# Kernel optimization log

Measured on AMD Instinct MI355X. Metric: run time of the kernel, lower is better.

Reference implementation:

```python
import jax, jax.numpy as jnp
import numpy as np

B, N, D = 8, 2048, 192
G, S = 512, 32
OUT = 384
ALPHA, BETA = 1000.0, 100.0
EPS = 1e-05


def setup_inputs() -> dict:
    key = jax.random.key(0)
    ks = jax.random.split(key, 8)
    sc = 0.02
    return {
        "points": jax.random.normal(ks[0], (B, N, 3), jnp.float32),
        "feats": jax.random.normal(ks[1], (B, N, D), jnp.float32),
        # 1x1 conv weights (BN assumed folded, inference form)
        "W1": sc * jax.random.normal(ks[2], (OUT, 2 * D), jnp.float32),
        "b1": jnp.zeros((OUT,), jnp.float32),
        "Wa": sc * jax.random.normal(ks[3], (OUT // 2, OUT), jnp.float32),
        "ba": jnp.zeros((OUT // 2,), jnp.float32),
        "Wb": sc * jax.random.normal(ks[4], (OUT, OUT // 2), jnp.float32),
        "bb": jnp.zeros((OUT,), jnp.float32),
    }


def fps(pts, n_samples):
    """Farthest point sampling. pts: (B,N,3) -> idx (B,n_samples) int32."""
    def one(p):  # (N,3)
        def step(carry, _):
            dists, last = carry
            cur = p[last]                                 # (3,)
            d = jnp.sum((p - cur) ** 2, axis=-1)          # (N,)
            dists = jnp.minimum(dists, d)
            nxt = jnp.argmax(dists).astype(jnp.int32)
            return (dists, nxt), last
        init = (jnp.full((p.shape[0],), jnp.inf, p.dtype), jnp.int32(0))
        _, idxs = jax.lax.scan(step, init, None, length=n_samples)
        return idxs
    return jax.vmap(one)(pts)


def pairwise_sqdist(a, b):
    # a: (B,G,3), b: (B,N,3) -> (B,G,N)
    aa = jnp.sum(a * a, -1)[:, :, None]
    bb = jnp.sum(b * b, -1)[:, None, :]
    return aa + bb - 2.0 * jnp.einsum('bgd,bnd->bgn', a, b)


def group_points(x, idx):
    # x: (B,N,C), idx: (B,G,S) -> (B,G,S,C)
    return jax.vmap(lambda f, i: f[i])(x, idx)


def pos_embed(xyz):
    # xyz: (B,G,S,3) -> (B,G,S,OUT)  Fourier positional encoding
    in_dim = xyz.shape[-1]
    feat_dim = OUT // (2 * in_dim)
    freq = jnp.arange(feat_dim, dtype=xyz.dtype)
    denom = jnp.power(jnp.asarray(ALPHA, xyz.dtype), freq / feat_dim)
    z = BETA * xyz[..., None] / denom                      # (B,G,S,3,feat_dim)
    pos = jnp.concatenate([jnp.sin(z), jnp.cos(z)], axis=-1)
    return pos.reshape(*xyz.shape[:-1], OUT)


def _forward(points, feats, W1, b1, Wa, ba, Wb, bb):
    # FPS centers
    fps_idx = fps(points, G)                               # (B,G)
    centers = jax.vmap(lambda p, i: p[i])(points, fps_idx)  # (B,G,3)

    d2 = pairwise_sqdist(centers, points)                  # (B,G,N)
    _, knn_idx = jax.lax.top_k(-d2, S)                     # (B,G,S)

    neighbor_pts = group_points(points, knn_idx)           # (B,G,S,3)
    neighbor_feats = group_points(feats, knn_idx)          # (B,G,S,D)

    # 'sim' normalization: global (scalar, unbiased) std of centered neighbors
    diff = neighbor_pts - centers[:, :, None, :]
    m = jnp.mean(diff)
    std = jnp.sqrt(jnp.sum((diff - m) ** 2) / (diff.size - 1))
    neighbor_pts = diff / (std + EPS)

    # center feats via 1-NN of centers in points
    center_idx = jnp.argmin(d2, axis=-1)                   # (B,G)
    center_feats = jax.vmap(lambda f, i: f[i])(feats, center_idx)  # (B,G,D)

    # concat neighbor + broadcast center feats -> (B,G,S,2D)
    gf = jnp.concatenate(
        [neighbor_feats, jnp.broadcast_to(center_feats[:, :, None, :], (points.shape[0], G, S, D))],
        axis=-1)

    # shared MLP (1x1 conv) + ReLU
    gf = jax.nn.relu(jnp.einsum('bgsc,oc->bgso', gf, W1) + b1)  # (B,G,S,OUT)

    pos = pos_embed(neighbor_pts)                          # (B,G,S,OUT)
    gf = (gf + pos) * pos

    # residual block: conv(OUT->OUT/2)+ReLU, conv(OUT/2->OUT), +x, ReLU
    h = jax.nn.relu(jnp.einsum('bgso,ho->bgsh', gf, Wa) + ba)
    h = jnp.einsum('bgsh,oh->bgso', h, Wb) + bb
    gf = jax.nn.relu(h + gf)

    # fused max + mean pooling over neighbors (S)
    out = jnp.max(gf, axis=2) + jnp.mean(gf, axis=2)       # (B,G,OUT)
    return centers, out


def reference(points, feats, W1, b1, Wa, ba, Wb, bb):
    return _forward(points, feats, W1, b1, Wa, ba, Wb, bb)
```

## Files before the change

### kernel.cpp

```cpp
#include <hip/hip_runtime.h>
#include <math.h>

#define Bn   8
#define Nn   2048
#define Dn   192
#define Gn   512
#define Sn   32
#define OUTn 384
#define Mrows (Bn * Gn * Sn)

typedef __attribute__((ext_vector_type(8))) unsigned short ushortx8;
typedef __attribute__((ext_vector_type(8))) __bf16 bf16x8;
typedef __attribute__((ext_vector_type(4))) float floatx4;

static constexpr size_t OFF_KNN    = 0;
static constexpr size_t OFF_CIDX   = 524288;
static constexpr size_t OFF_DIFF   = 540672;
static constexpr size_t OFF_SUMS   = 2113536;
static constexpr size_t OFF_STD    = 2113552;
static constexpr size_t OFF_CNT    = 2113568;
static constexpr size_t OFF_DENOM  = 2113792;
static constexpr size_t OFF_W1B    = 2114048;
static constexpr size_t OFF_WAB    = 2408960;
static constexpr size_t OFF_WBB    = 2556416;
static constexpr size_t OFF_G1     = 2703872;
static constexpr size_t OFF_FEATB  = 103367168;
static constexpr size_t OFF_CSTAGE = 109658624;

__device__ __forceinline__ unsigned short f2bf(float f) {
  unsigned u = __float_as_uint(f);
  unsigned r = (u + 0x7FFFu + ((u >> 16) & 1u)) >> 16;
  return (unsigned short)r;
}
__device__ __forceinline__ float bf2f(unsigned short h) {
  return __uint_as_float(((unsigned)h) << 16);
}
__device__ __forceinline__ floatx4 mfma_bf16(ushortx8 a, ushortx8 b, floatx4 c) {
  return __builtin_amdgcn_mfma_f32_16x16x32_bf16(
      __builtin_bit_cast(bf16x8, a), __builtin_bit_cast(bf16x8, b), c, 0, 0, 0);
}

__device__ __forceinline__ void gld16(const void* g, void* l) {
  __builtin_amdgcn_global_load_lds(
      (const __attribute__((address_space(1))) unsigned int*)g,
      (__attribute__((address_space(3))) unsigned int*)l, 16, 0, 0);
}

template <int CTRL>
__device__ __forceinline__ float dpp_max(float v) {
  int o = __builtin_amdgcn_update_dpp(0, __float_as_int(v), CTRL, 0xf, 0xf, true);
  return fmaxf(v, __int_as_float(o));
}

__global__ __launch_bounds__(256) void fused_front_kernel(
    const float* __restrict__ points, float* __restrict__ centers,
    const float* __restrict__ W1, const float* __restrict__ Wa,
    const float* __restrict__ Wb, const float* __restrict__ feats,
    unsigned short* __restrict__ W1b, unsigned short* __restrict__ Wab,
    unsigned short* __restrict__ Wbb, unsigned short* __restrict__ featb,
    float* __restrict__ rdenomTab, float* __restrict__ cstage,
    int* __restrict__ knn, int* __restrict__ cidx, float* __restrict__ diffb,
    double* __restrict__ sums, int* __restrict__ cnt, float* __restrict__ stdp) {
  const int t = threadIdx.x;
  const int w = t >> 6, lane = t & 63;

  if (blockIdx.x >= 8 && blockIdx.x < 8 + 3360) {
    const int base = (blockIdx.x - 8) * 1024 + t;
#pragma unroll
    for (int j = 0; j < 4; ++j) {
      const int i = base + j * 256;
      if (i < 147456)        W1b[i] = f2bf(W1[i]);
      else if (i < 221184)   Wab[i - 147456] = f2bf(Wa[i - 147456]);
      else if (i < 294912)   Wbb[i - 221184] = f2bf(Wb[i - 221184]);
      else                   featb[i - 294912] = f2bf(feats[i - 294912]);
    }
    if (blockIdx.x == 8 && t < 64)
      rdenomTab[t] = (float)(1.0 / pow(1000.0, (double)t / 64.0));
    return;
  }

  if (blockIdx.x >= 8 + 3360) {
    const int bg = (blockIdx.x - 3368) * 4 + w;
    const int b = bg >> 9;
    const float* P = points + (size_t)b * Nn * 3;
    const unsigned* cs = (const unsigned*)(cstage + (size_t)bg * 3);

    unsigned ux, uy, uz;
    for (;;) {
      ux = __hip_atomic_load(cs + 0, __ATOMIC_RELAXED, __HIP_MEMORY_SCOPE_AGENT);
      uy = __hip_atomic_load(cs + 1, __ATOMIC_RELAXED, __HIP_MEMORY_SCOPE_AGENT);
      uz = __hip_atomic_load(cs + 2, __ATOMIC_RELAXED, __HIP_MEMORY_SCOPE_AGENT);
      if (ux != 0xFFFFFFFFu && uy != 0xFFFFFFFFu && uz != 0xFFFFFFFFu) break;
      __builtin_amdgcn_s_sleep(16);
    }
    const float cx = __uint_as_float(ux);
    const float cy = __uint_as_float(uy);
    const float cz = __uint_as_float(uz);
    const float aa = __fadd_rn(__fadd_rn(__fmul_rn(cx, cx), __fmul_rn(cy, cy)), __fmul_rn(cz, cz));

    unsigned key[32];
#pragma unroll 8
    for (int s = 0; s < 32; ++s) {
      const int n = s * 64 + lane;
      float X = P[n * 3], Y = P[n * 3 + 1], Z = P[n * 3 + 2];
      float bbv = __fadd_rn(__fadd_rn(__fmul_rn(X, X), __fmul_rn(Y, Y)), __fmul_rn(Z, Z));
      float dot = __fadd_rn(__fadd_rn(__fmul_rn(cx, X), __fmul_rn(cy, Y)), __fmul_rn(cz, Z));
      float d2 = __fsub_rn(__fadd_rn(aa, bbv), __fmul_rn(2.0f, dot));
      unsigned u = __float_as_uint(d2);
      key[s] = u ^ ((unsigned)((int)u >> 31) | 0x80000000u);
    }

    unsigned mk = key[0]; int ms = 0;
#pragma unroll
    for (int s = 1; s < 32; ++s)
      if (key[s] < mk) { mk = key[s]; ms = s; }

    int mysel = 0;
    for (int it = 0; it < Sn; ++it) {
      unsigned long long p = ((unsigned long long)mk << 32) | (unsigned)(ms * 64 + lane);
#pragma unroll
      for (int off = 1; off <= 32; off <<= 1) {
        unsigned long long o = __shfl_xor(p, off, 64);
        p = (o < p) ? o : p;
      }
      const int n_win = (int)(unsigned)p;
      if (lane == it) mysel = n_win;
      if (lane == (n_win & 63)) {
        const int sw = n_win >> 6;
#pragma unroll
        for (int s = 0; s < 32; ++s)
          if (s == sw) key[s] = 0xFFFFFFFFu;
        mk = key[0]; ms = 0;
#pragma unroll
        for (int s = 1; s < 32; ++s)
          if (key[s] < mk) { mk = key[s]; ms = s; }
      }
    }

    double s1 = 0.0, s2 = 0.0;
    if (lane < Sn) {
      knn[(size_t)bg * Sn + lane] = mysel;
      float X = P[mysel * 3], Y = P[mysel * 3 + 1], Z = P[mysel * 3 + 2];
      float dx = __fsub_rn(X, cx), dy = __fsub_rn(Y, cy), dz = __fsub_rn(Z, cz);
      float* db = diffb + (size_t)bg * 96 + lane * 3;
      db[0] = dx; db[1] = dy; db[2] = dz;
      s1 = (double)dx + (double)dy + (double)dz;
      s2 = (double)dx * (double)dx + (double)dy * (double)dy + (double)dz * (double)dz;
    }
#pragma unroll
    for (int off = 1; off <= 32; off <<= 1) {
      s1 += __shfl_xor(s1, off, 64);
      s2 += __shfl_xor(s2, off, 64);
    }
    if (lane == 0) {
      cidx[bg] = __shfl(mysel, 0, 64);
      atomicAdd(sums, s1);
      atomicAdd(sums + 1, s2);
    }
    __threadfence();
    __syncthreads();
    if (t == 0) {
      const int old = atomicAdd(cnt, 1);
      if (old == (Bn * Gn / 4) - 1) {
        __threadfence();
        const double S1 = atomicAdd(sums, 0.0);
        const double S2 = atomicAdd(sums + 1, 0.0);
        const double n = (double)(Bn * Gn * Sn * 3);
        const double mean = S1 / n;
        const double var = (S2 - S1 * mean) / (n - 1.0);
        const float stdf = (float)sqrt(var) + 1e-5f;
        *stdp = (float)(1.0 / (double)stdf);
      }
    }
    return;
  }

  const int b = blockIdx.x;
  __shared__ float4 p4[Nn];
  __shared__ unsigned long long wkey[2][4];

  const float* P = points + (size_t)b * Nn * 3;
  for (int n = t; n < Nn; n += 256) {
    float x = P[n * 3], y = P[n * 3 + 1], z = P[n * 3 + 2];
    p4[n] = make_float4(x, y, z, 0.f);
  }
  __syncthreads();

  float rx[8], ry[8], rz[8], dist[8];
#pragma unroll
  for (int k = 0; k < 8; ++k) {
    float4 p = p4[t * 8 + k];
    rx[k] = p.x; ry[k] = p.y; rz[k] = p.z;
    dist[k] = INFINITY;
  }

  int cur = 0;
  for (int it = 0; it < Gn; ++it) {
    const float4 c = p4[cur];
    if (t == 0) {
      float* cd = centers + ((size_t)b * Gn + it) * 3;
      cd[0] = c.x; cd[1] = c.y; cd[2] = c.z;
      unsigned* cs = (unsigned*)(cstage + ((size_t)b * Gn + it) * 3);
      __hip_atomic_store(cs + 0, __float_as_uint(c.x), __ATOMIC_RELAXED, __HIP_MEMORY_SCOPE_AGENT);
      __hip_atomic_store(cs + 1, __float_as_uint(c.y), __ATOMIC_RELAXED, __HIP_MEMORY_SCOPE_AGENT);
      __hip_atomic_store(cs + 2, __float_as_uint(c.z), __ATOMIC_RELAXED, __HIP_MEMORY_SCOPE_AGENT);
    }
    float bv = -1.0f;
#pragma unroll
    for (int k = 0; k < 8; ++k) {
      float dx = __fsub_rn(rx[k], c.x);
      float dy = __fsub_rn(ry[k], c.y);
      float dz = __fsub_rn(rz[k], c.z);
      float d = __fadd_rn(__fadd_rn(__fmul_rn(dx, dx), __fmul_rn(dy, dy)), __fmul_rn(dz, dz));
      dist[k] = fminf(dist[k], d);
      bv = fmaxf(bv, dist[k]);
    }
    int li = 7;
#pragma unroll
    for (int k = 6; k >= 0; --k) li = (dist[k] == bv) ? k : li;

    float red = bv;
    red = dpp_max<0x111>(red);
    red = dpp_max<0x112>(red);
    red = dpp_max<0x114>(red);
    red = dpp_max<0x118>(red);
    red = dpp_max<0x142>(red);
    red = dpp_max<0x143>(red);
    const float M = __int_as_float(__builtin_amdgcn_readlane(__float_as_int(red), 63));

    unsigned long long msk = __ballot(bv == M);
    const int L = __ffsll((long long)msk) - 1;
    const int liL = __builtin_amdgcn_readlane(li, L);
    const int idx = (w * 64 + L) * 8 + liL;

    unsigned long long key =
        ((unsigned long long)__float_as_uint(M) << 32) | (unsigned)(0x7FFFFFFF - idx);
    if (lane == 0) wkey[it & 1][w] = key;
    __syncthreads();
    unsigned long long k0 = wkey[it & 1][0];
    unsigned long long k1 = wkey[it & 1][1];
    unsigned long long k2 = wkey[it & 1][2];
    unsigned long long k3 = wkey[it & 1][3];
    unsigned long long m01 = (k1 > k0) ? k1 : k0;
    unsigned long long m23 = (k3 > k2) ? k3 : k2;
    unsigned long long mm = (m23 > m01) ? m23 : m01;
    cur = 0x7FFFFFFF - (int)(unsigned)mm;
  }
}

__global__ __launch_bounds__(256) void gemm1_kernel(
    const unsigned short* __restrict__ featb, const unsigned short* __restrict__ W1b,
    const float* __restrict__ b1, const int* __restrict__ knn,
    const int* __restrict__ cidx, const float* __restrict__ diffb,
    const float* __restrict__ rstd_p, const float* __restrict__ rdenomTab,
    unsigned short* __restrict__ G1) {
  __shared__ unsigned short As[128 * 64];
  __shared__ unsigned short Bs[128 * 64];
  const int t = threadIdx.x;
  const int bm = blockIdx.x, bn = blockIdx.y;
  const int wid = t >> 6, lane = t & 63, quad = lane >> 4, c16 = lane & 15;
  const int wr = wid >> 1, wc = wid & 1;

  int aOffN[4], aOffC[4], bOff[4];
#pragma unroll
  for (int i = 0; i < 4; ++i) {
    const int slot = i * 256 + t;
    const int row = slot >> 3, segV = slot & 7;
    const int seg = segV ^ (row & 7);
    const int grow = bm * 128 + row;
    const int bg = grow >> 5, s = grow & 31, bb_ = bg >> 9;
    const int nidx = knn[(size_t)bg * Sn + s];
    const int ci = cidx[bg];
    aOffN[i] = (bb_ * Nn + nidx) * Dn + seg * 8;
    aOffC[i] = (bb_ * Nn + ci) * Dn + seg * 8;
    bOff[i] = (bn * 128 + row) * 384 + seg * 8;
  }

  floatx4 acc[4][4];
#pragma unroll
  for (int i = 0; i < 4; ++i)
#pragma unroll
    for (int j = 0; j < 4; ++j) acc[i][j] = (floatx4){0.f, 0.f, 0.f, 0.f};

  for (int kt = 0; kt < 6; ++kt) {
    const int kb = kt * 64;
#pragma unroll
    for (int i = 0; i < 4; ++i) {
      const unsigned short* srcA =
          (kt < 3) ? (featb + aOffN[i] + kb) : (featb + aOffC[i] + (kb - 192));
      gld16(srcA, &As[(i * 256 + wid * 64) * 8]);
      gld16(W1b + bOff[i] + kb, &Bs[(i * 256 + wid * 64) * 8]);
    }
    __syncthreads();
#pragma unroll
    for (int ks = 0; ks < 2; ++ks) {
      ushortx8 af[4], bf[4];
#pragma unroll
      for (int mt = 0; mt < 4; ++mt) {
        const int row = wr * 64 + mt * 16 + c16;
        const int seg = (ks * 4 + quad) ^ (row & 7);
        af[mt] = *(const ushortx8*)&As[row * 64 + seg * 8];
      }
#pragma unroll
      for (int nt = 0; nt < 4; ++nt) {
        const int row = wc * 64 + nt * 16 + c16;
        const int seg = (ks * 4 + quad) ^ (row & 7);
        bf[nt] = *(const ushortx8*)&Bs[row * 64 + seg * 8];
      }
#pragma unroll
      for (int mt = 0; mt < 4; ++mt)
#pragma unroll
        for (int nt = 0; nt < 4; ++nt)
          acc[mt][nt] = mfma_bf16(af[mt], bf[nt], acc[mt][nt]);
    }
    __syncthreads();
  }

  const float rstd = *rstd_p;
  float bias[4], rdnm[4];
  bool usin[4];
#pragma unroll
  for (int nt = 0; nt < 4; ++nt) {
    const int col = bn * 128 + wc * 64 + nt * 16 + c16;
    bias[nt] = b1[col];
    const int j = col & 127;
    usin[nt] = (j < 64);
    rdnm[nt] = rdenomTab[j & 63];
  }
#pragma unroll
  for (int mt = 0; mt < 4; ++mt) {
#pragma unroll
    for (int r = 0; r < 4; ++r) {
      const int row = bm * 128 + wr * 64 + mt * 16 + quad * 4 + r;
      const float dv = diffb[(size_t)row * 3 + bn];
      const float x = __fmul_rn(dv, rstd);
      const float zb = __fmul_rn(100.0f, x);
#pragma unroll
      for (int nt = 0; nt < 4; ++nt) {
        const int col = bn * 128 + wc * 64 + nt * 16 + c16;
        float y = fmaxf(acc[mt][nt][r] + bias[nt], 0.f);
        float z = __fmul_rn(zb, rdnm[nt]);
        float p = usin[nt] ? __sinf(z) : __cosf(z);
        float g = (y + p) * p;
        G1[(size_t)row * 384 + col] = f2bf(g);
      }
    }
  }
}

__global__ __launch_bounds__(512) void gemm23_kernel(
    const unsigned short* __restrict__ G1, const unsigned short* __restrict__ Wab,
    const float* __restrict__ ba, const unsigned short* __restrict__ Wbb,
    const float* __restrict__ bb, float* __restrict__ outp) {
  __shared__ __align__(16) char smem[100352];
  unsigned short* Htile = (unsigned short*)smem;
  unsigned short* As    = (unsigned short*)(smem + 51200);
  unsigned short* BsA   = (unsigned short*)(smem + 51200 + 16384);
  unsigned short* BsB   = (unsigned short*)(smem + 51200);

  const int t = threadIdx.x;
  const int bm = blockIdx.x;
  const int lane = t & 63, quad = lane >> 4, c16 = lane & 15;
  const int wid = t >> 6;
  const int wr = wid >> 2, wc = wid & 3;

  int aOff[2], bOffA[3];
#pragma unroll
  for (int i = 0; i < 2; ++i) {
    const int slot = i * 512 + t;
    const int row = slot >> 3, segV = slot & 7;
    aOff[i] = (bm * 128 + row) * 384 + (segV ^ (row & 7)) * 8;
  }
#pragma unroll
  for (int i = 0; i < 3; ++i) {
    const int slot = i * 512 + t;
    const int row = slot >> 3, segV = slot & 7;
    bOffA[i] = row * 384 + (segV ^ (row & 7)) * 8;
  }

  floatx4 accA[4][3];
#pragma unroll
  for (int i = 0; i < 4; ++i)
#pragma unroll
    for (int j = 0; j < 3; ++j) accA[i][j] = (floatx4){0.f, 0.f, 0.f, 0.f};

  for (int kt = 0; kt < 6; ++kt) {
    const int kb = kt * 64;
#pragma unroll
    for (int i = 0; i < 2; ++i) gld16(G1 + aOff[i] + kb, As + ((size_t)(i * 512 + t)) * 8);
#pragma unroll
    for (int i = 0; i < 3; ++i) gld16(Wab + bOffA[i] + kb, BsA + ((size_t)(i * 512 + t)) * 8);
    __syncthreads();
#pragma unroll
    for (int ks = 0; ks < 2; ++ks) {
      ushortx8 af[4], bf[3];
#pragma unroll
      for (int mt = 0; mt < 4; ++mt) {
        const int row = wr * 64 + mt * 16 + c16;
        const int seg = (ks * 4 + quad) ^ (row & 7);
        af[mt] = *(const ushortx8*)&As[row * 64 + seg * 8];
      }
#pragma unroll
      for (int nt = 0; nt < 3; ++nt) {
        const int row = wc * 48 + nt * 16 + c16;
        const int seg = (ks * 4 + quad) ^ (row & 7);
        bf[nt] = *(const ushortx8*)&BsA[row * 64 + seg * 8];
      }
#pragma unroll
      for (int mt = 0; mt < 4; ++mt)
#pragma unroll
        for (int nt = 0; nt < 3; ++nt)
          accA[mt][nt] = mfma_bf16(af[mt], bf[nt], accA[mt][nt]);
    }
    __syncthreads();
  }

#pragma unroll
  for (int nt = 0; nt < 3; ++nt) {
    const int col = wc * 48 + nt * 16 + c16;
    const float bias = ba[col];
#pragma unroll
    for (int mt = 0; mt < 4; ++mt)
#pragma unroll
      for (int r = 0; r < 4; ++r) {
        const int row = wr * 64 + mt * 16 + quad * 4 + r;
        Htile[row * 200 + col] = f2bf(fmaxf(accA[mt][nt][r] + bias, 0.f));
      }
  }
  __syncthreads();

  int bOffB[6];
#pragma unroll
  for (int i = 0; i < 6; ++i) {
    const int slot = i * 512 + t;
    const int row = slot >> 3, segV = slot & 7;
    bOffB[i] = row * 192 + (segV ^ (row & 7)) * 8;
  }

  floatx4 acc[4][6];
#pragma unroll
  for (int i = 0; i < 4; ++i)
#pragma unroll
    for (int j = 0; j < 6; ++j) acc[i][j] = (floatx4){0.f, 0.f, 0.f, 0.f};

  for (int kt = 0; kt < 3; ++kt) {
    const int kb = kt * 64;
#pragma unroll
    for (int i = 0; i < 6; ++i) gld16(Wbb + bOffB[i] + kb, BsB + ((size_t)(i * 512 + t)) * 8);
    __syncthreads();
#pragma unroll
    for (int ks = 0; ks < 2; ++ks) {
      ushortx8 af[4], bf[6];
#pragma unroll
      for (int mt = 0; mt < 4; ++mt) {
        const int row = wr * 64 + mt * 16 + c16;
        af[mt] = *(const ushortx8*)&Htile[row * 200 + kb + ks * 32 + quad * 8];
      }
#pragma unroll
      for (int nt = 0; nt < 6; ++nt) {
        const int row = wc * 96 + nt * 16 + c16;
        const int seg = (ks * 4 + quad) ^ (row & 7);
        bf[nt] = *(const ushortx8*)&BsB[row * 64 + seg * 8];
      }
#pragma unroll
      for (int mt = 0; mt < 4; ++mt)
#pragma unroll
        for (int nt = 0; nt < 6; ++nt)
          acc[mt][nt] = mfma_bf16(af[mt], bf[nt], acc[mt][nt]);
    }
    __syncthreads();
  }

#pragma unroll
  for (int nt = 0; nt < 6; ++nt) {
    const int col = wc * 96 + nt * 16 + c16;
    const float bias = bb[col];
    float gmax[2] = {-INFINITY, -INFINITY};
    float gsum[2] = {0.f, 0.f};
#pragma unroll
    for (int mt = 0; mt < 4; ++mt) {
      const int grp = mt >> 1;
#pragma unroll
      for (int r = 0; r < 4; ++r) {
        const int row = bm * 128 + wr * 64 + mt * 16 + quad * 4 + r;
        float v = acc[mt][nt][r] + bias + bf2f(G1[(size_t)row * 384 + col]);
        v = fmaxf(v, 0.f);
        gmax[grp] = fmaxf(gmax[grp], v);
        gsum[grp] += v;
      }
    }
#pragma unroll
    for (int grp = 0; grp < 2; ++grp) {
      float m = gmax[grp], su = gsum[grp];
#pragma unroll
      for (int off = 16; off <= 32; off <<= 1) {
        m = fmaxf(m, __shfl_xor(m, off, 64));
        su += __shfl_xor(su, off, 64);
      }
      if (quad == 0) {
        const int bg = bm * 4 + wr * 2 + grp;
        outp[(size_t)bg * 384 + col] = m + su / 32.0f;
      }
    }
  }
}

extern "C" void kernel_launch(void* const* d_in, const int* in_sizes, int n_in,
                              void* d_out, int out_size, void* d_ws, size_t ws_size,
                              hipStream_t stream) {
  const float* points = (const float*)d_in[0];
  const float* feats  = (const float*)d_in[1];
  const float* W1 = (const float*)d_in[2];
  const float* b1 = (const float*)d_in[3];
  const float* Wa = (const float*)d_in[4];
  const float* ba = (const float*)d_in[5];
  const float* Wb = (const float*)d_in[6];
  const float* bb = (const float*)d_in[7];
  float* outF = (float*)d_out;

  char* ws = (char*)d_ws;
  int*            knn      = (int*)(ws + OFF_KNN);
  int*            cidx     = (int*)(ws + OFF_CIDX);
  float*          diffb    = (float*)(ws + OFF_DIFF);
  double*         sums     = (double*)(ws + OFF_SUMS);
  float*          stdp     = (float*)(ws + OFF_STD);
  int*            cnt      = (int*)(ws + OFF_CNT);
  float*          rdenomTab= (float*)(ws + OFF_DENOM);
  unsigned short* W1b      = (unsigned short*)(ws + OFF_W1B);
  unsigned short* Wab      = (unsigned short*)(ws + OFF_WAB);
  unsigned short* Wbb      = (unsigned short*)(ws + OFF_WBB);
  unsigned short* G1       = (unsigned short*)(ws + OFF_G1);
  unsigned short* featb    = (unsigned short*)(ws + OFF_FEATB);
  float*          cstage   = (float*)(ws + OFF_CSTAGE);

  hipMemsetAsync(ws + OFF_SUMS, 0, 40, stream);
  hipMemsetAsync(ws + OFF_CSTAGE, 0xFF, (size_t)Bn * Gn * 3 * 4, stream);
  fused_front_kernel<<<8 + 3360 + 1024, 256, 0, stream>>>(
      points, outF, W1, Wa, Wb, feats, W1b, Wab, Wbb, featb, rdenomTab,
      cstage, knn, cidx, diffb, sums, cnt, stdp);
  gemm1_kernel<<<dim3(Mrows / 128, 3), 256, 0, stream>>>(featb, W1b, b1, knn, cidx,
                                                         diffb, stdp, rdenomTab, G1);
  gemm23_kernel<<<Mrows / 128, 512, 0, stream>>>(G1, Wab, ba, Wbb, bb, outF + Bn * Gn * 3);
}
```

Baseline: 459.8 us.

## Fuse gemm1 into front mega-kernel with flag-based producer/consumer sync

The separate gemm1 kernel becomes a third role inside the front kernel. GEMM1 tiles spin on per-group completion flags from the kNN blocks and on a prep-done counter, so their matrix work can overlap the serial FPS and kNN phases. The normalization step still waits for a global std value, which is published with a release store. The bf16 conversion prep is also vectorized to pack two values per 32-bit store, halving its block count. The cost is spin-waiting blocks holding CU slots, and correctness now depends on blocks being dispatched in index order to avoid deadlock.

```diff
diff --git a/kernel.cpp b/kernel.cpp
--- a/kernel.cpp
+++ b/kernel.cpp
@@ -9,6 +9,14 @@
 #define OUTn 384
 #define Mrows (Bn * Gn * Sn)
 
+#define NB_FPS   8
+#define NB_PREP  1680
+#define NB_KNN   1024
+#define NB_G1    3072
+#define BLK_PREP (NB_FPS)
+#define BLK_KNN  (NB_FPS + NB_PREP)
+#define BLK_G1   (NB_FPS + NB_PREP + NB_KNN)
+
 typedef __attribute__((ext_vector_type(8))) unsigned short ushortx8;
 typedef __attribute__((ext_vector_type(8))) __bf16 bf16x8;
 typedef __attribute__((ext_vector_type(4))) float floatx4;
@@ -19,6 +27,7 @@
 static constexpr size_t OFF_SUMS   = 2113536;
 static constexpr size_t OFF_STD    = 2113552;
 static constexpr size_t OFF_CNT    = 2113568;
+static constexpr size_t OFF_PCNT   = 2113572;
 static constexpr size_t OFF_DENOM  = 2113792;
 static constexpr size_t OFF_W1B    = 2114048;
 static constexpr size_t OFF_WAB    = 2408960;
@@ -26,6 +35,7 @@
 static constexpr size_t OFF_G1     = 2703872;
 static constexpr size_t OFF_FEATB  = 103367168;
 static constexpr size_t OFF_CSTAGE = 109658624;
+static constexpr size_t OFF_GFLAG  = 109707776;
 
 __device__ __forceinline__ unsigned short f2bf(float f) {
   unsigned u = __float_as_uint(f);
@@ -39,57 +49,80 @@
   return __builtin_amdgcn_mfma_f32_16x16x32_bf16(
       __builtin_bit_cast(bf16x8, a), __builtin_bit_cast(bf16x8, b), c, 0, 0, 0);
 }
-
 __device__ __forceinline__ void gld16(const void* g, void* l) {
   __builtin_amdgcn_global_load_lds(
       (const __attribute__((address_space(1))) unsigned int*)g,
       (__attribute__((address_space(3))) unsigned int*)l, 16, 0, 0);
 }
-
 template <int CTRL>
 __device__ __forceinline__ float dpp_max(float v) {
   int o = __builtin_amdgcn_update_dpp(0, __float_as_int(v), CTRL, 0xf, 0xf, true);
   return fmaxf(v, __int_as_float(o));
 }
-
-__global__ __launch_bounds__(256) void fused_front_kernel(
+__device__ __forceinline__ void ast_u32(unsigned* p, unsigned v) {
+  __hip_atomic_store(p, v, __ATOMIC_RELAXED, __HIP_MEMORY_SCOPE_AGENT);
+}
+__device__ __forceinline__ void ast_f32(float* p, float v) {
+  __hip_atomic_store(p, v, __ATOMIC_RELAXED, __HIP_MEMORY_SCOPE_AGENT);
+}
+__device__ __forceinline__ unsigned ald_u32(const unsigned* p) {
+  return __hip_atomic_load(p, __ATOMIC_RELAXED, __HIP_MEMORY_SCOPE_AGENT);
+}
+
+__global__ __launch_bounds__(256) void mega_kernel(
     const float* __restrict__ points, float* __restrict__ centers,
     const float* __restrict__ W1, const float* __restrict__ Wa,
     const float* __restrict__ Wb, const float* __restrict__ feats,
+    const float* __restrict__ b1,
     unsigned short* __restrict__ W1b, unsigned short* __restrict__ Wab,
     unsigned short* __restrict__ Wbb, unsigned short* __restrict__ featb,
     float* __restrict__ rdenomTab, float* __restrict__ cstage,
     int* __restrict__ knn, int* __restrict__ cidx, float* __restrict__ diffb,
-    double* __restrict__ sums, int* __restrict__ cnt, float* __restrict__ stdp) {
+    double* __restrict__ sums, int* __restrict__ cnt, unsigned* __restrict__ stdbits,
+    unsigned* __restrict__ pcnt, unsigned* __restrict__ gflag,
+    unsigned short* __restrict__ G1) {
   const int t = threadIdx.x;
   const int w = t >> 6, lane = t & 63;
-
-  if (blockIdx.x >= 8 && blockIdx.x < 8 + 3360) {
-    const int base = (blockIdx.x - 8) * 1024 + t;
+  const int blk = blockIdx.x;
+  __shared__ __align__(16) char smem[32832];
+
+  if (blk >= BLK_PREP && blk < BLK_KNN) {
+    unsigned* W1b32 = (unsigned*)W1b;
+    unsigned* Wab32 = (unsigned*)Wab;
+    unsigned* Wbb32 = (unsigned*)Wbb;
+    unsigned* fb32  = (unsigned*)featb;
+    const int base = (blk - BLK_PREP) * 1024 + t;
 #pragma unroll
     for (int j = 0; j < 4; ++j) {
       const int i = base + j * 256;
-      if (i < 147456)        W1b[i] = f2bf(W1[i]);
-      else if (i < 221184)   Wab[i - 147456] = f2bf(Wa[i - 147456]);
-      else if (i < 294912)   Wbb[i - 221184] = f2bf(Wb[i - 221184]);
-      else                   featb[i - 294912] = f2bf(feats[i - 294912]);
-    }
-    if (blockIdx.x == 8 && t < 64)
-      rdenomTab[t] = (float)(1.0 / pow(1000.0, (double)t / 64.0));
+      const float* src; unsigned* dst; int k;
+      if (i < 73728)       { src = W1;    dst = W1b32; k = i; }
+      else if (i < 110592) { src = Wa;    dst = Wab32; k = i - 73728; }
+      else if (i < 147456) { src = Wb;    dst = Wbb32; k = i - 110592; }
+      else                 { src = feats; dst = fb32;  k = i - 147456; }
+      const unsigned lo = f2bf(src[2 * k]);
+      const unsigned hi = f2bf(src[2 * k + 1]);
+      ast_u32(dst + k, lo | (hi << 16));
+    }
+    if (blk == BLK_PREP && t < 64)
+      ast_f32(rdenomTab + t, (float)(1.0 / pow(1000.0, (double)t / 64.0)));
+    __syncthreads();
+    if (t == 0) {
+      __threadfence();
+      __hip_atomic_fetch_add(pcnt, 1u, __ATOMIC_RELEASE, __HIP_MEMORY_SCOPE_AGENT);
+    }
     return;
   }
 
-  if (blockIdx.x >= 8 + 3360) {
-    const int bg = (blockIdx.x - 3368) * 4 + w;
+  if (blk >= BLK_KNN && blk < BLK_G1) {
+    const int bg = (blk - BLK_KNN) * 4 + w;
     const int b = bg >> 9;
     const float* P = points + (size_t)b * Nn * 3;
     const unsigned* cs = (const unsigned*)(cstage + (size_t)bg * 3);
 
     unsigned ux, uy, uz;
     for (;;) {
-      ux = __hip_atomic_load(cs + 0, __ATOMIC_RELAXED, __HIP_MEMORY_SCOPE_AGENT);
-      uy = __hip_atomic_load(cs + 1, __ATOMIC_RELAXED, __HIP_MEMORY_SCOPE_AGENT);
-      uz = __hip_atomic_load(cs + 2, __ATOMIC_RELAXED, __HIP_MEMORY_SCOPE_AGENT);
+      ux = ald_u32(cs + 0); uy = ald_u32(cs + 1); uz = ald_u32(cs + 2);
       if (ux != 0xFFFFFFFFu && uy != 0xFFFFFFFFu && uz != 0xFFFFFFFFu) break;
       __builtin_amdgcn_s_sleep(16);
     }
@@ -109,7 +142,6 @@
       unsigned u = __float_as_uint(d2);
       key[s] = u ^ ((unsigned)((int)u >> 31) | 0x80000000u);
     }
-
     unsigned mk = key[0]; int ms = 0;
 #pragma unroll
     for (int s = 1; s < 32; ++s)
@@ -139,11 +171,11 @@
 
     double s1 = 0.0, s2 = 0.0;
     if (lane < Sn) {
-      knn[(size_t)bg * Sn + lane] = mysel;
+      ast_u32((unsigned*)&knn[(size_t)bg * Sn + lane], (unsigned)mysel);
       float X = P[mysel * 3], Y = P[mysel * 3 + 1], Z = P[mysel * 3 + 2];
       float dx = __fsub_rn(X, cx), dy = __fsub_rn(Y, cy), dz = __fsub_rn(Z, cz);
       float* db = diffb + (size_t)bg * 96 + lane * 3;
-      db[0] = dx; db[1] = dy; db[2] = dz;
+      ast_f32(db + 0, dx); ast_f32(db + 1, dy); ast_f32(db + 2, dz);
       s1 = (double)dx + (double)dy + (double)dz;
       s2 = (double)dx * (double)dx + (double)dy * (double)dy + (double)dz * (double)dz;
     }
@@ -153,15 +185,16 @@
       s2 += __shfl_xor(s2, off, 64);
     }
     if (lane == 0) {
-      cidx[bg] = __shfl(mysel, 0, 64);
+      ast_u32((unsigned*)&cidx[bg], (unsigned)__shfl(mysel, 0, 64));
       atomicAdd(sums, s1);
       atomicAdd(sums + 1, s2);
+      __hip_atomic_store(&gflag[bg], 1u, __ATOMIC_RELEASE, __HIP_MEMORY_SCOPE_AGENT);
     }
     __threadfence();
     __syncthreads();
     if (t == 0) {
       const int old = atomicAdd(cnt, 1);
-      if (old == (Bn * Gn / 4) - 1) {
+      if (old == NB_KNN - 1) {
         __threadfence();
         const double S1 = atomicAdd(sums, 0.0);
         const double S2 = atomicAdd(sums + 1, 0.0);
@@ -169,15 +202,129 @@
         const double mean = S1 / n;
         const double var = (S2 - S1 * mean) / (n - 1.0);
         const float stdf = (float)sqrt(var) + 1e-5f;
-        *stdp = (float)(1.0 / (double)stdf);
+        const float rstdv = (float)(1.0 / (double)stdf);
+        __hip_atomic_store(stdbits, __float_as_uint(rstdv), __ATOMIC_RELEASE,
+                           __HIP_MEMORY_SCOPE_AGENT);
       }
     }
     return;
   }
 
-  const int b = blockIdx.x;
-  __shared__ float4 p4[Nn];
-  __shared__ unsigned long long wkey[2][4];
+  if (blk >= BLK_G1) {
+    const int gb = blk - BLK_G1;
+    const int bm = gb & 1023, bn = gb >> 10;
+    unsigned short* As = (unsigned short*)smem;
+    unsigned short* Bs = (unsigned short*)(smem + 16384);
+    const int wid = w, quad = lane >> 4, c16 = lane & 15;
+    const int wr = wid >> 1, wc = wid & 1;
+
+    while (__hip_atomic_load(pcnt, __ATOMIC_ACQUIRE, __HIP_MEMORY_SCOPE_AGENT) <
+           (unsigned)NB_PREP)
+      __builtin_amdgcn_s_sleep(32);
+#pragma unroll
+    for (int g = 0; g < 4; ++g)
+      while (__hip_atomic_load(&gflag[bm * 4 + g], __ATOMIC_ACQUIRE,
+                               __HIP_MEMORY_SCOPE_AGENT) == 0u)
+        __builtin_amdgcn_s_sleep(16);
+
+    int aOffN[4], aOffC[4], bOff[4];
+#pragma unroll
+    for (int i = 0; i < 4; ++i) {
+      const int slot = i * 256 + t;
+      const int row = slot >> 3, segV = slot & 7;
+      const int seg = segV ^ (row & 7);
+      const int grow = bm * 128 + row;
+      const int bg = grow >> 5, s = grow & 31, bb_ = bg >> 9;
+      const int nidx = knn[(size_t)bg * Sn + s];
+      const int ci = (int)ald_u32((const unsigned*)&cidx[bg]);
+      aOffN[i] = (bb_ * Nn + nidx) * Dn + seg * 8;
+      aOffC[i] = (bb_ * Nn + ci) * Dn + seg * 8;
+      bOff[i] = (bn * 128 + row) * 384 + seg * 8;
+    }
+
+    floatx4 acc[4][4];
+#pragma unroll
+    for (int i = 0; i < 4; ++i)
+#pragma unroll
+      for (int j = 0; j < 4; ++j) acc[i][j] = (floatx4){0.f, 0.f, 0.f, 0.f};
+
+    for (int kt = 0; kt < 6; ++kt) {
+      const int kb = kt * 64;
+#pragma unroll
+      for (int i = 0; i < 4; ++i) {
+        const unsigned short* srcA =
+            (kt < 3) ? (featb + aOffN[i] + kb) : (featb + aOffC[i] + (kb - 192));
+        gld16(srcA, &As[(i * 256 + wid * 64) * 8]);
+        gld16(W1b + bOff[i] + kb, &Bs[(i * 256 + wid * 64) * 8]);
+      }
+      __syncthreads();
+#pragma unroll
+      for (int ks = 0; ks < 2; ++ks) {
+        ushortx8 af[4], bf[4];
+#pragma unroll
+        for (int mt = 0; mt < 4; ++mt) {
+          const int row = wr * 64 + mt * 16 + c16;
+          const int seg = (ks * 4 + quad) ^ (row & 7);
+          af[mt] = *(const ushortx8*)&As[row * 64 + seg * 8];
+        }
+#pragma unroll
+        for (int nt = 0; nt < 4; ++nt) {
+          const int row = wc * 64 + nt * 16 + c16;
+          const int seg = (ks * 4 + quad) ^ (row & 7);
+          bf[nt] = *(const ushortx8*)&Bs[row * 64 + seg * 8];
+        }
+#pragma unroll
+        for (int mt = 0; mt < 4; ++mt)
+#pragma unroll
+          for (int nt = 0; nt < 4; ++nt)
+            acc[mt][nt] = mfma_bf16(af[mt], bf[nt], acc[mt][nt]);
+      }
+      __syncthreads();
+    }
+
+    unsigned sb;
+    for (;;) {
+      sb = __hip_atomic_load(stdbits, __ATOMIC_ACQUIRE, __HIP_MEMORY_SCOPE_AGENT);
+      if (sb != 0xFFFFFFFFu) break;
+      __builtin_amdgcn_s_sleep(16);
+    }
+    const float rstd = __uint_as_float(sb);
+
+    float bias[4], rdnm[4];
+    bool usin[4];
+#pragma unroll
+    for (int nt = 0; nt < 4; ++nt) {
+      const int col = bn * 128 + wc * 64 + nt * 16 + c16;
+      bias[nt] = b1[col];
+      const int j = col & 127;
+      usin[nt] = (j < 64);
+      rdnm[nt] = rdenomTab[j & 63];
+    }
+#pragma unroll
+    for (int mt = 0; mt < 4; ++mt) {
+#pragma unroll
+      for (int r = 0; r < 4; ++r) {
+        const int row = bm * 128 + wr * 64 + mt * 16 + quad * 4 + r;
+        const float dv = diffb[(size_t)row * 3 + bn];
+        const float x = __fmul_rn(dv, rstd);
+        const float zb = __fmul_rn(100.0f, x);
+#pragma unroll
+        for (int nt = 0; nt < 4; ++nt) {
+          const int col = bn * 128 + wc * 64 + nt * 16 + c16;
+          float y = fmaxf(acc[mt][nt][r] + bias[nt], 0.f);
+          float z = __fmul_rn(zb, rdnm[nt]);
+          float p = usin[nt] ? __sinf(z) : __cosf(z);
+          float g = (y + p) * p;
+          G1[(size_t)row * 384 + col] = f2bf(g);
+        }
+      }
+    }
+    return;
+  }
+
+  const int b = blk;
+  float4* p4 = (float4*)smem;
+  unsigned long long* wkey = (unsigned long long*)(smem + 32768);
 
   const float* P = points + (size_t)b * Nn * 3;
   for (int n = t; n < Nn; n += 256) {
@@ -201,9 +348,9 @@
       float* cd = centers + ((size_t)b * Gn + it) * 3;
       cd[0] = c.x; cd[1] = c.y; cd[2] = c.z;
       unsigned* cs = (unsigned*)(cstage + ((size_t)b * Gn + it) * 3);
-      __hip_atomic_store(cs + 0, __float_as_uint(c.x), __ATOMIC_RELAXED, __HIP_MEMORY_SCOPE_AGENT);
-      __hip_atomic_store(cs + 1, __float_as_uint(c.y), __ATOMIC_RELAXED, __HIP_MEMORY_SCOPE_AGENT);
-      __hip_atomic_store(cs + 2, __float_as_uint(c.z), __ATOMIC_RELAXED, __HIP_MEMORY_SCOPE_AGENT);
+      ast_u32(cs + 0, __float_as_uint(c.x));
+      ast_u32(cs + 1, __float_as_uint(c.y));
+      ast_u32(cs + 2, __float_as_uint(c.z));
     }
     float bv = -1.0f;
 #pragma unroll
@@ -235,116 +382,16 @@
 
     unsigned long long key =
         ((unsigned long long)__float_as_uint(M) << 32) | (unsigned)(0x7FFFFFFF - idx);
-    if (lane == 0) wkey[it & 1][w] = key;
-    __syncthreads();
-    unsigned long long k0 = wkey[it & 1][0];
-    unsigned long long k1 = wkey[it & 1][1];
-    unsigned long long k2 = wkey[it & 1][2];
-    unsigned long long k3 = wkey[it & 1][3];
+    if (lane == 0) wkey[(it & 1) * 4 + w] = key;
+    __syncthreads();
+    unsigned long long k0 = wkey[(it & 1) * 4 + 0];
+    unsigned long long k1 = wkey[(it & 1) * 4 + 1];
+    unsigned long long k2 = wkey[(it & 1) * 4 + 2];
+    unsigned long long k3 = wkey[(it & 1) * 4 + 3];
     unsigned long long m01 = (k1 > k0) ? k1 : k0;
     unsigned long long m23 = (k3 > k2) ? k3 : k2;
     unsigned long long mm = (m23 > m01) ? m23 : m01;
     cur = 0x7FFFFFFF - (int)(unsigned)mm;
-  }
-}
-
-__global__ __launch_bounds__(256) void gemm1_kernel(
-    const unsigned short* __restrict__ featb, const unsigned short* __restrict__ W1b,
-    const float* __restrict__ b1, const int* __restrict__ knn,
-    const int* __restrict__ cidx, const float* __restrict__ diffb,
-    const float* __restrict__ rstd_p, const float* __restrict__ rdenomTab,
-    unsigned short* __restrict__ G1) {
-  __shared__ unsigned short As[128 * 64];
-  __shared__ unsigned short Bs[128 * 64];
-  const int t = threadIdx.x;
-  const int bm = blockIdx.x, bn = blockIdx.y;
-  const int wid = t >> 6, lane = t & 63, quad = lane >> 4, c16 = lane & 15;
-  const int wr = wid >> 1, wc = wid & 1;
-
-  int aOffN[4], aOffC[4], bOff[4];
-#pragma unroll
-  for (int i = 0; i < 4; ++i) {
-    const int slot = i * 256 + t;
-    const int row = slot >> 3, segV = slot & 7;
-    const int seg = segV ^ (row & 7);
-    const int grow = bm * 128 + row;
-    const int bg = grow >> 5, s = grow & 31, bb_ = bg >> 9;
-    const int nidx = knn[(size_t)bg * Sn + s];
-    const int ci = cidx[bg];
-    aOffN[i] = (bb_ * Nn + nidx) * Dn + seg * 8;
-    aOffC[i] = (bb_ * Nn + ci) * Dn + seg * 8;
-    bOff[i] = (bn * 128 + row) * 384 + seg * 8;
-  }
-
-  floatx4 acc[4][4];
-#pragma unroll
-  for (int i = 0; i < 4; ++i)
-#pragma unroll
-    for (int j = 0; j < 4; ++j) acc[i][j] = (floatx4){0.f, 0.f, 0.f, 0.f};
-
-  for (int kt = 0; kt < 6; ++kt) {
-    const int kb = kt * 64;
-#pragma unroll
-    for (int i = 0; i < 4; ++i) {
-      const unsigned short* srcA =
-          (kt < 3) ? (featb + aOffN[i] + kb) : (featb + aOffC[i] + (kb - 192));
-      gld16(srcA, &As[(i * 256 + wid * 64) * 8]);
-      gld16(W1b + bOff[i] + kb, &Bs[(i * 256 + wid * 64) * 8]);
-    }
-    __syncthreads();
-#pragma unroll
-    for (int ks = 0; ks < 2; ++ks) {
-      ushortx8 af[4], bf[4];
-#pragma unroll
-      for (int mt = 0; mt < 4; ++mt) {
-        const int row = wr * 64 + mt * 16 + c16;
-        const int seg = (ks * 4 + quad) ^ (row & 7);
-        af[mt] = *(const ushortx8*)&As[row * 64 + seg * 8];
-      }
-#pragma unroll
-      for (int nt = 0; nt < 4; ++nt) {
-        const int row = wc * 64 + nt * 16 + c16;
-        const int seg = (ks * 4 + quad) ^ (row & 7);
-        bf[nt] = *(const ushortx8*)&Bs[row * 64 + seg * 8];
-      }
-#pragma unroll
-      for (int mt = 0; mt < 4; ++mt)
-#pragma unroll
-        for (int nt = 0; nt < 4; ++nt)
-          acc[mt][nt] = mfma_bf16(af[mt], bf[nt], acc[mt][nt]);
-    }
-    __syncthreads();
-  }
-
-  const float rstd = *rstd_p;
-  float bias[4], rdnm[4];
-  bool usin[4];
-#pragma unroll
-  for (int nt = 0; nt < 4; ++nt) {
-    const int col = bn * 128 + wc * 64 + nt * 16 + c16;
-    bias[nt] = b1[col];
-    const int j = col & 127;
-    usin[nt] = (j < 64);
-    rdnm[nt] = rdenomTab[j & 63];
-  }
-#pragma unroll
-  for (int mt = 0; mt < 4; ++mt) {
-#pragma unroll
-    for (int r = 0; r < 4; ++r) {
-      const int row = bm * 128 + wr * 64 + mt * 16 + quad * 4 + r;
-      const float dv = diffb[(size_t)row * 3 + bn];
-      const float x = __fmul_rn(dv, rstd);
-      const float zb = __fmul_rn(100.0f, x);
-#pragma unroll
-      for (int nt = 0; nt < 4; ++nt) {
-        const int col = bn * 128 + wc * 64 + nt * 16 + c16;
-        float y = fmaxf(acc[mt][nt][r] + bias[nt], 0.f);
-        float z = __fmul_rn(zb, rdnm[nt]);
-        float p = usin[nt] ? __sinf(z) : __cosf(z);
-        float g = (y + p) * p;
-        G1[(size_t)row * 384 + col] = f2bf(g);
-      }
-    }
   }
 }
 
@@ -523,8 +570,9 @@
   int*            cidx     = (int*)(ws + OFF_CIDX);
   float*          diffb    = (float*)(ws + OFF_DIFF);
   double*         sums     = (double*)(ws + OFF_SUMS);
-  float*          stdp     = (float*)(ws + OFF_STD);
+  unsigned*       stdbits  = (unsigned*)(ws + OFF_STD);
   int*            cnt      = (int*)(ws + OFF_CNT);
+  unsigned*       pcnt     = (unsigned*)(ws + OFF_PCNT);
   float*          rdenomTab= (float*)(ws + OFF_DENOM);
   unsigned short* W1b      = (unsigned short*)(ws + OFF_W1B);
   unsigned short* Wab      = (unsigned short*)(ws + OFF_WAB);
@@ -532,13 +580,14 @@
   unsigned short* G1       = (unsigned short*)(ws + OFF_G1);
   unsigned short* featb    = (unsigned short*)(ws + OFF_FEATB);
   float*          cstage   = (float*)(ws + OFF_CSTAGE);
+  unsigned*       gflag    = (unsigned*)(ws + OFF_GFLAG);
 
   hipMemsetAsync(ws + OFF_SUMS, 0, 40, stream);
+  hipMemsetAsync(ws + OFF_STD, 0xFF, 4, stream);
   hipMemsetAsync(ws + OFF_CSTAGE, 0xFF, (size_t)Bn * Gn * 3 * 4, stream);
-  fused_front_kernel<<<8 + 3360 + 1024, 256, 0, stream>>>(
-      points, outF, W1, Wa, Wb, feats, W1b, Wab, Wbb, featb, rdenomTab,
-      cstage, knn, cidx, diffb, sums, cnt, stdp);
-  gemm1_kernel<<<dim3(Mrows / 128, 3), 256, 0, stream>>>(featb, W1b, b1, knn, cidx,
-                                                         diffb, stdp, rdenomTab, G1);
+  hipMemsetAsync(ws + OFF_GFLAG, 0, (size_t)Bn * Gn * 4, stream);
+  mega_kernel<<<NB_FPS + NB_PREP + NB_KNN + NB_G1, 256, 0, stream>>>(
+      points, outF, W1, Wa, Wb, feats, b1, W1b, Wab, Wbb, featb, rdenomTab,
+      cstage, knn, cidx, diffb, sums, cnt, stdbits, pcnt, gflag, G1);
   gemm23_kernel<<<Mrows / 128, 512, 0, stream>>>(G1, Wab, ba, Wbb, bb, outF + Bn * Gn * 3);
 }
```

Measured after the change: 1.093 ms. 2.38x slower.
